# Optimization experiments

Hardware: AMD Instinct MI355X
Metric: run time of the kernel (lower is better)

Reference implementation:

```python
import jax, jax.numpy as jnp
import numpy as np

N_USER, N_ITEM, N_REL = 200000, 100000, 64
DIM = 64
S_UU = S_UI = S_IU = S_II = 8
BATCH = 65536
MAX_RATING = 5.0


def setup_inputs() -> dict:
    key = jax.random.key(0)
    ks = jax.random.split(key, 24)
    inp = {}
    # query batch
    inp['u'] = jax.random.randint(ks[0], (BATCH,), 0, N_USER)
    inp['v'] = jax.random.randint(ks[1], (BATCH,), 0, N_ITEM)
    # embedding tables (init std=0.8 as in the torch code)
    inp['usr_feat'] = 0.8 * jax.random.normal(ks[2], (N_USER, DIM), jnp.float32)
    inp['item_feat'] = 0.8 * jax.random.normal(ks[3], (N_ITEM, DIM), jnp.float32)
    inp['rel_feat'] = 0.8 * jax.random.normal(ks[4], (N_REL, DIM), jnp.float32)
    # precomputed sampled neighbor tables (built once in __init__ in the original)
    inp['neigh_uu'] = jax.random.randint(ks[5], (N_USER, S_UU), 0, N_USER)
    inp['neigh_uu_st'] = jax.random.uniform(ks[6], (N_USER, S_UU), jnp.float32)
    inp['neigh_ui'] = jax.random.randint(ks[7], (N_USER, S_UI), 0, N_ITEM)
    inp['neigh_ui_rat'] = MAX_RATING * jax.random.uniform(ks[8], (N_USER, S_UI), jnp.float32)
    inp['neigh_ui_vot'] = jax.random.uniform(ks[9], (N_USER, S_UI), jnp.float32)
    inp['neigh_ui_tim'] = jax.random.uniform(ks[10], (N_USER, S_UI), jnp.float32)
    inp['neigh_iu'] = jax.random.randint(ks[11], (N_ITEM, S_IU), 0, N_USER)
    inp['neigh_iu_rat'] = MAX_RATING * jax.random.uniform(ks[12], (N_ITEM, S_IU), jnp.float32)
    inp['neigh_iu_vot'] = jax.random.uniform(ks[13], (N_ITEM, S_IU), jnp.float32)
    inp['neigh_iu_tim'] = jax.random.uniform(ks[14], (N_ITEM, S_IU), jnp.float32)
    inp['neigh_ii'] = jax.random.randint(ks[15], (N_ITEM, S_II), 0, N_ITEM)
    inp['neigh_ir'] = jax.random.randint(ks[16], (N_ITEM, S_II), 0, N_REL)
    # aggregator transforms (one per side)
    sc = 1.0 / np.sqrt(DIM)
    inp['Wu'] = sc * jax.random.normal(ks[17], (DIM, DIM), jnp.float32)
    inp['bu'] = jnp.zeros((DIM,), jnp.float32)
    inp['Wv'] = sc * jax.random.normal(ks[18], (DIM, DIM), jnp.float32)
    inp['bv'] = jnp.zeros((DIM,), jnp.float32)
    return inp


def reference(u, v, usr_feat, item_feat, rel_feat,
              neigh_uu, neigh_uu_st, neigh_ui, neigh_ui_rat, neigh_ui_vot, neigh_ui_tim,
              neigh_iu, neigh_iu_rat, neigh_iu_vot, neigh_iu_tim, neigh_ii, neigh_ir,
              Wu, bu, Wv, bv):
    u_emb = usr_feat[u]                                   # [B, D]
    v_emb = item_feat[v]                                  # [B, D]

    # ---- user-side aggregation ----
    # social neighbors, weighted by softmax over social tie strength
    uu_nei = usr_feat[neigh_uu[u]]                        # [B, S, D]
    w_uu = jax.nn.softmax(neigh_uu_st[u], axis=-1)        # [B, S]
    agg_uu = jnp.einsum('bs,bsd->bd', w_uu, uu_nei)
    # interacted items, weighted by rating * vote * time recency
    ui_nei = item_feat[neigh_ui[u]]                       # [B, S, D]
    s_ui = neigh_ui_rat[u] * neigh_ui_vot[u] * neigh_ui_tim[u]
    w_ui = jax.nn.softmax(s_ui, axis=-1)
    agg_ui = jnp.einsum('bs,bsd->bd', w_ui, ui_nei)
    user_h = jax.nn.relu((u_emb + agg_uu + agg_ui) @ Wu + bu)

    # ---- item-side aggregation ----
    # users who interacted with the item, weighted like above
    iu_nei = usr_feat[neigh_iu[v]]                        # [B, S, D]
    s_iu = neigh_iu_rat[v] * neigh_iu_vot[v] * neigh_iu_tim[v]
    w_iu = jax.nn.softmax(s_iu, axis=-1)
    agg_iu = jnp.einsum('bs,bsd->bd', w_iu, iu_nei)
    # KG neighbors with user-relation attention (KGCN-style)
    ii_nei = item_feat[neigh_ii[v]]                       # [B, S, D]
    rel = rel_feat[neigh_ir[v]]                           # [B, S, D]
    att = jnp.einsum('bd,bsd->bs', u_emb, rel)            # user-relation score
    w_ii = jax.nn.softmax(att, axis=-1)
    agg_ii = jnp.einsum('bs,bsd->bd', w_ii, ii_nei)
    item_h = jax.nn.relu((v_emb + agg_iu + agg_ii) @ Wv + bv)

    # rating prediction
    score = jax.nn.sigmoid(jnp.sum(user_h * item_h, axis=-1)) * MAX_RATING
    return score
```

## Files before the change

kernel.cpp:

```cpp
#include <hip/hip_runtime.h>
#include <math.h>

constexpr int DIM = 64;
constexpr int S = 8;
constexpr int WPB = 16;
constexpr int BLOCK = WPB * 64;
constexpr int GRID = 512;
constexpr int BSTR = 33;

template <int CTRL>
__device__ __forceinline__ float dppx(float x) {
    return __builtin_bit_cast(float,
        __builtin_amdgcn_mov_dpp(__builtin_bit_cast(int, x), CTRL, 0xf, 0xf, true));
}
#define XOR1 0xB1
#define XOR2 0x4E

__device__ __forceinline__ unsigned pk_bf16(float a, float b) {
    unsigned ua = __builtin_bit_cast(unsigned, a);
    unsigned ub = __builtin_bit_cast(unsigned, b);
    ua = (ua + 0x8000u) >> 16;
    ub = (ub + 0x8000u) & 0xffff0000u;
    return ua | ub;
}

__device__ __forceinline__ void octet_softmax(float sc, float* wout) {
    float m = sc;
    m = fmaxf(m, dppx<XOR1>(m));
    m = fmaxf(m, dppx<XOR2>(m));
    m = fmaxf(m, __shfl_xor(m, 4));
    float e = __expf(sc - m);
    float s = e;
    s += dppx<XOR1>(s);
    s += dppx<XOR2>(s);
    s += __shfl_xor(s, 4);
    float w = e / s;
    #pragma unroll
    for (int k = 0; k < 8; k++) wout[k] = __shfl(w, k);
}

__global__ __launch_bounds__(BLOCK)
void sestkgcn_kernel(
    const int*   __restrict__ u_idx,
    const int*   __restrict__ v_idx,
    const float* __restrict__ usr_feat,
    const float* __restrict__ item_feat,
    const float* __restrict__ rel_feat,
    const int*   __restrict__ neigh_uu,
    const float* __restrict__ neigh_uu_st,
    const int*   __restrict__ neigh_ui,
    const float* __restrict__ neigh_ui_rat,
    const float* __restrict__ neigh_ui_vot,
    const float* __restrict__ neigh_ui_tim,
    const int*   __restrict__ neigh_iu,
    const float* __restrict__ neigh_iu_rat,
    const float* __restrict__ neigh_iu_vot,
    const float* __restrict__ neigh_iu_tim,
    const int*   __restrict__ neigh_ii,
    const int*   __restrict__ neigh_ir,
    const float* __restrict__ Wu,
    const float* __restrict__ bu,
    const float* __restrict__ Wv,
    const float* __restrict__ bv,
    float*       __restrict__ out,
    int n)
{
    __shared__ unsigned sWuP[DIM * BSTR];
    __shared__ unsigned sWvP[DIM * BSTR];
    __shared__ float sbu[DIM];
    __shared__ float sbv[DIM];
    __shared__ float xs[WPB * DIM];

    const int tid = threadIdx.x;
    for (int i = tid; i < DIM * 32; i += BLOCK) {
        const int j_ = i & 63, m_ = i >> 6;
        sWuP[j_ * BSTR + m_] = pk_bf16(Wu[m_ * DIM + j_], Wu[(m_ + 32) * DIM + j_]);
        sWvP[j_ * BSTR + m_] = pk_bf16(Wv[m_ * DIM + j_], Wv[(m_ + 32) * DIM + j_]);
    }
    if (tid < DIM) { sbu[tid] = bu[tid]; sbv[tid] = bv[tid]; }
    __syncthreads();

    const int wave = tid >> 6;
    const int lane = tid & 63;
    const int ls   = lane & 7;

    float* xw = &xs[wave * DIM];
    const unsigned* wuP = &sWuP[lane * BSTR];
    const unsigned* wvP = &sWvP[lane * BSTR];
    const float4* xw4 = (const float4*)xw;
    const float bu_l = sbu[lane];
    const float bv_l = sbv[lane];

    const int stride = GRID * WPB;
    int b = blockIdx.x * WPB + wave;
    if (b >= n) return;

    int u = u_idx[b];
    int v = v_idx[b];

    while (b < n) {
        const int b2 = b + stride;
        const int bc = (b2 < n) ? b2 : b;
        const int u_nxt = u_idx[bc];
        const int v_nxt = v_idx[bc];

        const unsigned u8 = (unsigned)u << 3, v8 = (unsigned)v << 3;

        const float u_d = usr_feat[((unsigned)u << 6) | (unsigned)lane];
        const float v_d = item_feat[((unsigned)v << 6) | (unsigned)lane];

        const float sc_uu = neigh_uu_st[u8 + ls];
        const float sc_ui = neigh_ui_rat[u8 + ls] * neigh_ui_vot[u8 + ls] * neigh_ui_tim[u8 + ls];
        const float sc_iu = neigh_iu_rat[v8 + ls] * neigh_iu_vot[v8 + ls] * neigh_iu_tim[v8 + ls];

        float w[S];
        octet_softmax(sc_uu, w);
        float agg_uu = 0.f;
        {
            const int4 i0 = ((const int4*)(neigh_uu + u8))[0];
            const int4 i1 = ((const int4*)(neigh_uu + u8))[1];
            const int ni[S] = {i0.x, i0.y, i0.z, i0.w, i1.x, i1.y, i1.z, i1.w};
            float r[S];
            #pragma unroll
            for (int s = 0; s < S; s++) r[s] = usr_feat[((unsigned)ni[s] << 6) | (unsigned)lane];
            #pragma unroll
            for (int s = 0; s < S; s++) agg_uu = fmaf(w[s], r[s], agg_uu);
        }

        octet_softmax(sc_ui, w);
        float agg_ui = 0.f;
        {
            const int4 i0 = ((const int4*)(neigh_ui + u8))[0];
            const int4 i1 = ((const int4*)(neigh_ui + u8))[1];
            const int ni[S] = {i0.x, i0.y, i0.z, i0.w, i1.x, i1.y, i1.z, i1.w};
            float r[S];
            #pragma unroll
            for (int s = 0; s < S; s++) r[s] = item_feat[((unsigned)ni[s] << 6) | (unsigned)lane];
            #pragma unroll
            for (int s = 0; s < S; s++) agg_ui = fmaf(w[s], r[s], agg_ui);
        }

        float hu;
        {
            xw[lane] = u_d + agg_uu + agg_ui;
            __threadfence_block();
            float a0 = 0.f, a1 = 0.f;
            #pragma unroll
            for (int k = 0; k < 8; k++) {
                const float4 xa = xw4[k];
                const float4 xb = xw4[k + 8];
                #pragma unroll
                for (int t = 0; t < 4; t++) {
                    const unsigned wd = wuP[4 * k + t];
                    const float wlo = __builtin_bit_cast(float, wd << 16);
                    const float whi = __builtin_bit_cast(float, wd & 0xffff0000u);
                    const float xat = (t == 0) ? xa.x : (t == 1) ? xa.y : (t == 2) ? xa.z : xa.w;
                    const float xbt = (t == 0) ? xb.x : (t == 1) ? xb.y : (t == 2) ? xb.z : xb.w;
                    a0 = fmaf(xat, wlo, a0);
                    a1 = fmaf(xbt, whi, a1);
                }
            }
            hu = fmaxf(a0 + a1 + bu_l, 0.f);
        }

        octet_softmax(sc_iu, w);
        float agg_iu = 0.f;
        {
            const int4 i0 = ((const int4*)(neigh_iu + v8))[0];
            const int4 i1 = ((const int4*)(neigh_iu + v8))[1];
            const int ni[S] = {i0.x, i0.y, i0.z, i0.w, i1.x, i1.y, i1.z, i1.w};
            float r[S];
            #pragma unroll
            for (int s = 0; s < S; s++) r[s] = usr_feat[((unsigned)ni[s] << 6) | (unsigned)lane];
            #pragma unroll
            for (int s = 0; s < S; s++) agg_iu = fmaf(w[s], r[s], agg_iu);
        }

        {
            const int4 r0 = ((const int4*)(neigh_ir + v8))[0];
            const int4 r1 = ((const int4*)(neigh_ir + v8))[1];
            const int nr[S] = {r0.x, r0.y, r0.z, r0.w, r1.x, r1.y, r1.z, r1.w};
            float p[S];
            #pragma unroll
            for (int s = 0; s < S; s++) p[s] = u_d * rel_feat[((unsigned)nr[s] << 6) | (unsigned)lane];

            float m1[4];
            #pragma unroll
            for (int i = 0; i < 4; i++) {
                float lo = (lane & 1) ? p[2 * i + 1] : p[2 * i];
                float hi = (lane & 1) ? p[2 * i]     : p[2 * i + 1];
                m1[i] = lo + dppx<XOR1>(hi);
            }
            float m2[2];
            #pragma unroll
            for (int i = 0; i < 2; i++) {
                float lo = (lane & 2) ? m1[2 * i + 1] : m1[2 * i];
                float hi = (lane & 2) ? m1[2 * i]     : m1[2 * i + 1];
                m2[i] = lo + dppx<XOR2>(hi);
            }
            float lo = (lane & 4) ? m2[1] : m2[0];
            float hi = (lane & 4) ? m2[0] : m2[1];
            float att = lo + __shfl_xor(hi, 4);
            att += __shfl_xor(att, 8);
            att += __shfl_xor(att, 16);
            att += __shfl_xor(att, 32);
            octet_softmax(att, w);
        }
        float agg_ii = 0.f;
        {
            const int4 i0 = ((const int4*)(neigh_ii + v8))[0];
            const int4 i1 = ((const int4*)(neigh_ii + v8))[1];
            const int ni[S] = {i0.x, i0.y, i0.z, i0.w, i1.x, i1.y, i1.z, i1.w};
            float r[S];
            #pragma unroll
            for (int s = 0; s < S; s++) r[s] = item_feat[((unsigned)ni[s] << 6) | (unsigned)lane];
            #pragma unroll
            for (int s = 0; s < S; s++) agg_ii = fmaf(w[s], r[s], agg_ii);
        }

        float hv;
        {
            __threadfence_block();
            xw[lane] = v_d + agg_iu + agg_ii;
            __threadfence_block();
            float a0 = 0.f, a1 = 0.f;
            #pragma unroll
            for (int k = 0; k < 8; k++) {
                const float4 xa = xw4[k];
                const float4 xb = xw4[k + 8];
                #pragma unroll
                for (int t = 0; t < 4; t++) {
                    const unsigned wd = wvP[4 * k + t];
                    const float wlo = __builtin_bit_cast(float, wd << 16);
                    const float whi = __builtin_bit_cast(float, wd & 0xffff0000u);
                    const float xat = (t == 0) ? xa.x : (t == 1) ? xa.y : (t == 2) ? xa.z : xa.w;
                    const float xbt = (t == 0) ? xb.x : (t == 1) ? xb.y : (t == 2) ? xb.z : xb.w;
                    a0 = fmaf(xat, wlo, a0);
                    a1 = fmaf(xbt, whi, a1);
                }
            }
            hv = fmaxf(a0 + a1 + bv_l, 0.f);
        }

        float p = hu * hv;
        p += dppx<XOR1>(p);
        p += dppx<XOR2>(p);
        p += __shfl_xor(p, 4);
        p += __shfl_xor(p, 8);
        p += __shfl_xor(p, 16);
        p += __shfl_xor(p, 32);
        if (lane == 0) out[b] = 5.0f / (1.0f + __expf(-p));

        b = b2;
        u = u_nxt;
        v = v_nxt;
    }
}

extern "C" void kernel_launch(void* const* d_in, const int* in_sizes, int n_in,
                              void* d_out, int out_size, void* d_ws, size_t ws_size,
                              hipStream_t stream) {
    const int*   u_idx        = (const int*)  d_in[0];
    const int*   v_idx        = (const int*)  d_in[1];
    const float* usr_feat     = (const float*)d_in[2];
    const float* item_feat    = (const float*)d_in[3];
    const float* rel_feat     = (const float*)d_in[4];
    const int*   neigh_uu     = (const int*)  d_in[5];
    const float* neigh_uu_st  = (const float*)d_in[6];
    const int*   neigh_ui     = (const int*)  d_in[7];
    const float* neigh_ui_rat = (const float*)d_in[8];
    const float* neigh_ui_vot = (const float*)d_in[9];
    const float* neigh_ui_tim = (const float*)d_in[10];
    const int*   neigh_iu     = (const int*)  d_in[11];
    const float* neigh_iu_rat = (const float*)d_in[12];
    const float* neigh_iu_vot = (const float*)d_in[13];
    const float* neigh_iu_tim = (const float*)d_in[14];
    const int*   neigh_ii     = (const int*)  d_in[15];
    const int*   neigh_ir     = (const int*)  d_in[16];
    const float* Wu           = (const float*)d_in[17];
    const float* bu           = (const float*)d_in[18];
    const float* Wv           = (const float*)d_in[19];
    const float* bv           = (const float*)d_in[20];
    float*       out          = (float*)d_out;

    const int n = in_sizes[0];
    int blocks = (n + WPB - 1) / WPB;
    if (blocks > GRID) blocks = GRID;
    sestkgcn_kernel<<<blocks, BLOCK, 0, stream>>>(
        u_idx, v_idx, usr_feat, item_feat, rel_feat,
        neigh_uu, neigh_uu_st, neigh_ui, neigh_ui_rat, neigh_ui_vot, neigh_ui_tim,
        neigh_iu, neigh_iu_rat, neigh_iu_vot, neigh_iu_tim, neigh_ii, neigh_ir,
        Wu, bu, Wv, bv, out, n);
}
```

Measured before the change: 249.3 us.

## Compute per-row projections with MFMA bf16 using hi/lo split of activations

Replaces the per-lane scalar FMA matvec (64x64 bf16 weights in LDS) with MFMA 16x16x32 bf16 instructions. The activation vector is split into high and low bf16 parts to keep near-fp32 accuracy, and the weights are repacked in LDS in MFMA fragment layout. Only row 0 of the MFMA output is used, so most of the matrix unit's work is wasted. The launch bounds also add a minimum-occupancy hint, which may constrain registers.

```diff
diff --git a/kernel.cpp b/kernel.cpp
--- a/kernel.cpp
+++ b/kernel.cpp
@@ -6,7 +6,11 @@
 constexpr int WPB = 16;
 constexpr int BLOCK = WPB * 64;
 constexpr int GRID = 512;
-constexpr int BSTR = 33;
+
+typedef __attribute__((ext_vector_type(8))) __bf16 bf16x8;
+typedef __attribute__((ext_vector_type(4))) float  f32x4;
+
+#define LDS_FENCE() asm volatile("s_waitcnt lgkmcnt(0)" ::: "memory")
 
 template <int CTRL>
 __device__ __forceinline__ float dppx(float x) {
@@ -39,7 +43,63 @@
     for (int k = 0; k < 8; k++) wout[k] = __shfl(w, k);
 }
 
-__global__ __launch_bounds__(BLOCK)
+__device__ __forceinline__ void matvec_h(
+    float xv, int lane, unsigned short* xw,
+    const bf16x8* xa00, const bf16x8* xa01,
+    const bf16x8* xa10, const bf16x8* xa11,
+    const unsigned* bf,
+    float b0, float b1, float b2, float b3,
+    float& h0, float& h1, float& h2, float& h3)
+{
+    LDS_FENCE();
+    const unsigned xb = __builtin_bit_cast(unsigned, xv);
+    const unsigned hb = (xb + 0x8000u) & 0xffff0000u;
+    const float xl = xv - __builtin_bit_cast(float, hb);
+    xw[lane]      = (unsigned short)(hb >> 16);
+    xw[64 + lane] = (unsigned short)((__builtin_bit_cast(unsigned, xl) + 0x8000u) >> 16);
+    LDS_FENCE();
+
+    f32x4 a0 = {0.f, 0.f, 0.f, 0.f};
+    f32x4 a1 = a0, a2 = a0, a3 = a0;
+
+    {
+        const bf16x8 ah = *xa00, al = *xa01;
+        const bf16x8 w0 = *(const bf16x8*)(bf);
+        const bf16x8 w1 = *(const bf16x8*)(bf + 256);
+        const bf16x8 w2 = *(const bf16x8*)(bf + 512);
+        const bf16x8 w3 = *(const bf16x8*)(bf + 768);
+        a0 = __builtin_amdgcn_mfma_f32_16x16x32_bf16(ah, w0, a0, 0, 0, 0);
+        a0 = __builtin_amdgcn_mfma_f32_16x16x32_bf16(al, w0, a0, 0, 0, 0);
+        a1 = __builtin_amdgcn_mfma_f32_16x16x32_bf16(ah, w1, a1, 0, 0, 0);
+        a1 = __builtin_amdgcn_mfma_f32_16x16x32_bf16(al, w1, a1, 0, 0, 0);
+        a2 = __builtin_amdgcn_mfma_f32_16x16x32_bf16(ah, w2, a2, 0, 0, 0);
+        a2 = __builtin_amdgcn_mfma_f32_16x16x32_bf16(al, w2, a2, 0, 0, 0);
+        a3 = __builtin_amdgcn_mfma_f32_16x16x32_bf16(ah, w3, a3, 0, 0, 0);
+        a3 = __builtin_amdgcn_mfma_f32_16x16x32_bf16(al, w3, a3, 0, 0, 0);
+    }
+    {
+        const bf16x8 ah = *xa10, al = *xa11;
+        const bf16x8 w0 = *(const bf16x8*)(bf + 1024);
+        const bf16x8 w1 = *(const bf16x8*)(bf + 1280);
+        const bf16x8 w2 = *(const bf16x8*)(bf + 1536);
+        const bf16x8 w3 = *(const bf16x8*)(bf + 1792);
+        a0 = __builtin_amdgcn_mfma_f32_16x16x32_bf16(ah, w0, a0, 0, 0, 0);
+        a0 = __builtin_amdgcn_mfma_f32_16x16x32_bf16(al, w0, a0, 0, 0, 0);
+        a1 = __builtin_amdgcn_mfma_f32_16x16x32_bf16(ah, w1, a1, 0, 0, 0);
+        a1 = __builtin_amdgcn_mfma_f32_16x16x32_bf16(al, w1, a1, 0, 0, 0);
+        a2 = __builtin_amdgcn_mfma_f32_16x16x32_bf16(ah, w2, a2, 0, 0, 0);
+        a2 = __builtin_amdgcn_mfma_f32_16x16x32_bf16(al, w2, a2, 0, 0, 0);
+        a3 = __builtin_amdgcn_mfma_f32_16x16x32_bf16(ah, w3, a3, 0, 0, 0);
+        a3 = __builtin_amdgcn_mfma_f32_16x16x32_bf16(al, w3, a3, 0, 0, 0);
+    }
+
+    h0 = fmaxf(a0[0] + b0, 0.f);
+    h1 = fmaxf(a1[0] + b1, 0.f);
+    h2 = fmaxf(a2[0] + b2, 0.f);
+    h3 = fmaxf(a3[0] + b3, 0.f);
+}
+
+__global__ __launch_bounds__(BLOCK, 4)
 void sestkgcn_kernel(
     const int*   __restrict__ u_idx,
     const int*   __restrict__ v_idx,
@@ -65,31 +125,36 @@
     float*       __restrict__ out,
     int n)
 {
-    __shared__ unsigned sWuP[DIM * BSTR];
-    __shared__ unsigned sWvP[DIM * BSTR];
-    __shared__ float sbu[DIM];
-    __shared__ float sbv[DIM];
-    __shared__ float xs[WPB * DIM];
+    __shared__ unsigned sBFu[2048];
+    __shared__ unsigned sBFv[2048];
+    __shared__ __align__(16) unsigned short sX[WPB][128];
 
     const int tid = threadIdx.x;
-    for (int i = tid; i < DIM * 32; i += BLOCK) {
-        const int j_ = i & 63, m_ = i >> 6;
-        sWuP[j_ * BSTR + m_] = pk_bf16(Wu[m_ * DIM + j_], Wu[(m_ + 32) * DIM + j_]);
-        sWvP[j_ * BSTR + m_] = pk_bf16(Wv[m_ * DIM + j_], Wv[(m_ + 32) * DIM + j_]);
+    for (int i = tid; i < 2048; i += BLOCK) {
+        const int d = i & 3, l = (i >> 2) & 63, f = i >> 8;
+        const int row = ((f >> 2) << 5) + ((l >> 4) << 3) + (d << 1);
+        const int col = ((f & 3) << 4) + (l & 15);
+        sBFu[i] = pk_bf16(Wu[row * DIM + col], Wu[(row + 1) * DIM + col]);
+        sBFv[i] = pk_bf16(Wv[row * DIM + col], Wv[(row + 1) * DIM + col]);
     }
-    if (tid < DIM) { sbu[tid] = bu[tid]; sbv[tid] = bv[tid]; }
     __syncthreads();
 
     const int wave = tid >> 6;
     const int lane = tid & 63;
     const int ls   = lane & 7;
-
-    float* xw = &xs[wave * DIM];
-    const unsigned* wuP = &sWuP[lane * BSTR];
-    const unsigned* wvP = &sWvP[lane * BSTR];
-    const float4* xw4 = (const float4*)xw;
-    const float bu_l = sbu[lane];
-    const float bv_l = sbv[lane];
+    const int g    = lane >> 4;
+    const int c    = lane & 15;
+
+    unsigned short* xw = &sX[wave][0];
+    const bf16x8* xa00 = (const bf16x8*)&sX[wave][g * 8];
+    const bf16x8* xa01 = (const bf16x8*)&sX[wave][64 + g * 8];
+    const bf16x8* xa10 = (const bf16x8*)&sX[wave][32 + g * 8];
+    const bf16x8* xa11 = (const bf16x8*)&sX[wave][96 + g * 8];
+    const unsigned* bfu = &sBFu[lane * 4];
+    const unsigned* bfv = &sBFv[lane * 4];
+
+    const float bu0 = bu[c], bu1 = bu[c + 16], bu2 = bu[c + 32], bu3 = bu[c + 48];
+    const float bv0 = bv[c], bv1 = bv[c + 16], bv2 = bv[c + 32], bv3 = bv[c + 48];
 
     const int stride = GRID * WPB;
     int b = blockIdx.x * WPB + wave;
@@ -140,28 +205,9 @@
             for (int s = 0; s < S; s++) agg_ui = fmaf(w[s], r[s], agg_ui);
         }
 
-        float hu;
-        {
-            xw[lane] = u_d + agg_uu + agg_ui;
-            __threadfence_block();
-            float a0 = 0.f, a1 = 0.f;
-            #pragma unroll
-            for (int k = 0; k < 8; k++) {
-                const float4 xa = xw4[k];
-                const float4 xb = xw4[k + 8];
-                #pragma unroll
-                for (int t = 0; t < 4; t++) {
-                    const unsigned wd = wuP[4 * k + t];
-                    const float wlo = __builtin_bit_cast(float, wd << 16);
-                    const float whi = __builtin_bit_cast(float, wd & 0xffff0000u);
-                    const float xat = (t == 0) ? xa.x : (t == 1) ? xa.y : (t == 2) ? xa.z : xa.w;
-                    const float xbt = (t == 0) ? xb.x : (t == 1) ? xb.y : (t == 2) ? xb.z : xb.w;
-                    a0 = fmaf(xat, wlo, a0);
-                    a1 = fmaf(xbt, whi, a1);
-                }
-            }
-            hu = fmaxf(a0 + a1 + bu_l, 0.f);
-        }
+        float hu0, hu1, hu2, hu3;
+        matvec_h(u_d + agg_uu + agg_ui, lane, xw, xa00, xa01, xa10, xa11,
+                 bfu, bu0, bu1, bu2, bu3, hu0, hu1, hu2, hu3);
 
         octet_softmax(sc_iu, w);
         float agg_iu = 0.f;
@@ -218,37 +264,15 @@
             for (int s = 0; s < S; s++) agg_ii = fmaf(w[s], r[s], agg_ii);
         }
 
-        float hv;
-        {
-            __threadfence_block();
-            xw[lane] = v_d + agg_iu + agg_ii;
-            __threadfence_block();
-            float a0 = 0.f, a1 = 0.f;
-            #pragma unroll
-            for (int k = 0; k < 8; k++) {
-                const float4 xa = xw4[k];
-                const float4 xb = xw4[k + 8];
-                #pragma unroll
-                for (int t = 0; t < 4; t++) {
-                    const unsigned wd = wvP[4 * k + t];
-                    const float wlo = __builtin_bit_cast(float, wd << 16);
-                    const float whi = __builtin_bit_cast(float, wd & 0xffff0000u);
-                    const float xat = (t == 0) ? xa.x : (t == 1) ? xa.y : (t == 2) ? xa.z : xa.w;
-                    const float xbt = (t == 0) ? xb.x : (t == 1) ? xb.y : (t == 2) ? xb.z : xb.w;
-                    a0 = fmaf(xat, wlo, a0);
-                    a1 = fmaf(xbt, whi, a1);
-                }
-            }
-            hv = fmaxf(a0 + a1 + bv_l, 0.f);
-        }
-
-        float p = hu * hv;
+        float hv0, hv1, hv2, hv3;
+        matvec_h(v_d + agg_iu + agg_ii, lane, xw, xa00, xa01, xa10, xa11,
+                 bfv, bv0, bv1, bv2, bv3, hv0, hv1, hv2, hv3);
+
+        float p = hu0 * hv0 + hu1 * hv1 + hu2 * hv2 + hu3 * hv3;
         p += dppx<XOR1>(p);
         p += dppx<XOR2>(p);
         p += __shfl_xor(p, 4);
         p += __shfl_xor(p, 8);
-        p += __shfl_xor(p, 16);
-        p += __shfl_xor(p, 32);
         if (lane == 0) out[b] = 5.0f / (1.0f + __expf(-p));
 
         b = b2;
```

Result: no change. 248.0 us (-0.5%).
